# Kernel tuning notes

Hardware: AMD Instinct MI355X
Metric: run time of the kernel (lower is better)

## Reference

```python
import jax, jax.numpy as jnp
import numpy as np


def _compact_positions(mask, K):
    """mask: [B, T] bool. Returns [B, K] with the (ascending) indices t where
    mask[b, t] is True, compacted to the front; remaining slots are -1.
    Stable argsort on ~mask puts True positions first, preserving order.
    """
    order = jnp.argsort(jnp.logical_not(mask), axis=1, stable=True)  # [B, T]
    counts = mask.sum(axis=1, keepdims=True)                          # [B, 1]
    pos = order[:, :K]                                                # [B, K]
    valid = jnp.arange(K)[None, :] < jnp.minimum(counts, K)
    return jnp.where(valid, pos, -1)


def setup_inputs() -> dict:
    key = jax.random.key(0)
    k_r, k_e = jax.random.split(key)
    B, MAX_ROUTING, D = 16, 4096, 512
    routing = jax.random.randint(k_r, (B, MAX_ROUTING), 0, 2, dtype=jnp.int32)
    pos_embed = jax.random.normal(k_e, (MAX_ROUTING, D), dtype=jnp.float32)
    return {"routing": routing, "max_nodes": 1024, "max_edges": 2048,
            "pos_embed": pos_embed}


def reference(routing, max_nodes, max_edges, pos_embed):
    # Compacted logical positions of node tokens (routing==0) and edge tokens
    # (routing==1), replacing the sequential per-batch Python loop.
    node_pos = _compact_positions(routing == 0, max_nodes)  # [B, max_nodes]
    edge_pos = _compact_positions(routing == 1, max_edges)  # [B, max_edges]

    # Each node spans 2 tokens, each edge spans 5 tokens:
    # unsqueeze(-1).repeat(...,k).view == elementwise repeat along axis 1.
    node_tok = jnp.repeat(node_pos, 2, axis=1)  # [B, max_nodes*2]
    edge_tok = jnp.repeat(edge_pos, 5, axis=1)  # [B, max_edges*5]

    node_pe = pos_embed[jnp.maximum(node_tok, 0)]  # [B, max_nodes*2, D]
    edge_pe = pos_embed[jnp.maximum(edge_tok, 0)]  # [B, max_edges*5, D]
    return node_pe, edge_pe
```

## Files before the change

kernel.cpp:

```cpp
#include <hip/hip_runtime.h>

#define NB 16
#define NT 4096
#define ND 512
#define ND4 128
#define MAX_NODES 1024
#define MAX_EDGES 2048
#define NODE_ROWS 2048
#define EDGE_ROWS 10240
#define ROWS_NODE_TOT 32768u
#define ROWS_TOTAL 196608u

typedef __attribute__((ext_vector_type(4))) float f4;

__global__ __launch_bounds__(1024) void compact_kernel(
    const int* __restrict__ routing,
    int* __restrict__ node_pos,
    int* __restrict__ edge_pos)
{
    const int b   = blockIdx.x;
    const int tid = threadIdx.x;
    const int lane = tid & 63;
    const int wv   = tid >> 6;

    const int4 v = reinterpret_cast<const int4*>(routing + b * NT)[tid];
    const int e0 = v.x, e1 = v.y, e2 = v.z, e3 = v.w;

    unsigned inc0 = ((e0 == 0) ? 0x10000u : 0u) | ((e0 == 1) ? 1u : 0u);
    unsigned inc1 = ((e1 == 0) ? 0x10000u : 0u) | ((e1 == 1) ? 1u : 0u);
    unsigned inc2 = ((e2 == 0) ? 0x10000u : 0u) | ((e2 == 1) ? 1u : 0u);
    unsigned inc3 = ((e3 == 0) ? 0x10000u : 0u) | ((e3 == 1) ? 1u : 0u);
    unsigned p0 = inc0;
    unsigned p1 = p0 + inc1;
    unsigned p2 = p1 + inc2;
    unsigned p3 = p2 + inc3;
    const unsigned my_sum = p3;

    unsigned x = my_sum;
    #pragma unroll
    for (int off = 1; off < 64; off <<= 1) {
        unsigned y = __shfl_up(x, off, 64);
        if (lane >= off) x += y;
    }

    __shared__ unsigned wave_sums[16];
    if (lane == 63) wave_sums[wv] = x;

    node_pos[b * MAX_NODES + tid] = -1;
    edge_pos[b * MAX_EDGES + 2 * tid + 0] = -1;
    edge_pos[b * MAX_EDGES + 2 * tid + 1] = -1;
    __syncthreads();

    unsigned offset = 0;
    for (int i = 0; i < wv; ++i) offset += wave_sums[i];

    const unsigned base = offset + x - my_sum;

    const unsigned ex0 = base;
    const unsigned ex1 = base + p0;
    const unsigned ex2 = base + p1;
    const unsigned ex3 = base + p2;

    const int t0 = tid * 4;
    #pragma unroll 4
    for (int i = 0; i < 4; ++i) {
        const int      e  = (i == 0) ? e0 : (i == 1) ? e1 : (i == 2) ? e2 : e3;
        const unsigned ex = (i == 0) ? ex0 : (i == 1) ? ex1 : (i == 2) ? ex2 : ex3;
        if (e == 0) {
            const unsigned rank = ex >> 16;
            if (rank < MAX_NODES) node_pos[b * MAX_NODES + rank] = t0 + i;
        } else if (e == 1) {
            const unsigned rank = ex & 0xFFFFu;
            if (rank < MAX_EDGES) edge_pos[b * MAX_EDGES + rank] = t0 + i;
        }
    }
}

__global__ __launch_bounds__(256) void gather_fused_kernel(
    const float4* __restrict__ pe,
    const int* __restrict__ node_pos,
    const int* __restrict__ edge_pos,
    float4* __restrict__ out)
{
    const unsigned gid = blockIdx.x * 256u + threadIdx.x;
    const unsigned row = gid >> 6;
    const unsigned t   = gid & 63u;

    int tok;
    if (row < ROWS_NODE_TOT) {
        const unsigned b = row >> 11;
        const unsigned j = row & 2047u;
        tok = node_pos[b * MAX_NODES + (j >> 1)];
    } else {
        const unsigned r2 = row - ROWS_NODE_TOT;
        const unsigned b  = r2 / EDGE_ROWS;
        const unsigned j  = r2 - b * EDGE_ROWS;
        tok = edge_pos[b * MAX_EDGES + j / 5u];
    }
    const int src = tok < 0 ? 0 : tok;

    const f4* srcp = (const f4*)(pe + (size_t)src * ND4);
    f4* dstp       = (f4*)(out + (size_t)row * ND4);

    const f4 v0 = srcp[t];
    const f4 v1 = srcp[t + 64];
    __builtin_nontemporal_store(v0, dstp + t);
    __builtin_nontemporal_store(v1, dstp + t + 64);
}

extern "C" void kernel_launch(void* const* d_in, const int* in_sizes, int n_in,
                              void* d_out, int out_size, void* d_ws, size_t ws_size,
                              hipStream_t stream) {
    const int*   routing = (const int*)d_in[0];
    const float* pe      = (const float*)d_in[3];

    int* node_pos = (int*)d_ws;
    int* edge_pos = node_pos + NB * MAX_NODES;

    compact_kernel<<<NB, 1024, 0, stream>>>(routing, node_pos, edge_pos);

    const unsigned total_threads = ROWS_TOTAL * 64u;
    gather_fused_kernel<<<total_threads / 256, 256, 0, stream>>>(
        (const float4*)pe, node_pos, edge_pos, (float4*)d_out);
}
```

Measured before the change: 404.2 us.

## Fuse compaction and gather into one kernel with redundant per-block scan

Merges the compaction kernel and the gather kernel into a single launch. Each of 512 blocks recomputes its batch's prefix-scan compaction into LDS, then gathers its slice of node and edge rows. This removes the second launch, the inter-kernel dependency and the workspace round trip. In exchange, each batch's scan is repeated 32 times, and the grid shrinks to 512 blocks of 1024 threads, which may lower the memory parallelism available for the roughly 400MB write stream.

```diff
diff --git a/kernel.cpp b/kernel.cpp
--- a/kernel.cpp
+++ b/kernel.cpp
@@ -2,26 +2,34 @@
 
 #define NB 16
 #define NT 4096
-#define ND 512
 #define ND4 128
 #define MAX_NODES 1024
 #define MAX_EDGES 2048
 #define NODE_ROWS 2048
 #define EDGE_ROWS 10240
 #define ROWS_NODE_TOT 32768u
-#define ROWS_TOTAL 196608u
+#define SUBS 32
+#define NBLK (NB * SUBS)
+#define NODE_ROWS_PER_BLK 64u
+#define EDGE_ROWS_PER_BLK 320u
 
 typedef __attribute__((ext_vector_type(4))) float f4;
 
-__global__ __launch_bounds__(1024) void compact_kernel(
+__global__ __launch_bounds__(1024) void fused_pe_kernel(
     const int* __restrict__ routing,
-    int* __restrict__ node_pos,
-    int* __restrict__ edge_pos)
+    const f4*  __restrict__ pe,
+    f4*        __restrict__ out)
 {
-    const int b   = blockIdx.x;
-    const int tid = threadIdx.x;
+    const unsigned blk = blockIdx.x;
+    const unsigned b   = blk >> 5;
+    const unsigned sub = blk & 31u;
+    const int tid  = threadIdx.x;
     const int lane = tid & 63;
     const int wv   = tid >> 6;
+
+    __shared__ int      node_lds[MAX_NODES];
+    __shared__ int      edge_lds[MAX_EDGES];
+    __shared__ unsigned wave_sums[16];
 
     const int4 v = reinterpret_cast<const int4*>(routing + b * NT)[tid];
     const int e0 = v.x, e1 = v.y, e2 = v.z, e3 = v.w;
@@ -42,18 +50,15 @@
         unsigned y = __shfl_up(x, off, 64);
         if (lane >= off) x += y;
     }
-
-    __shared__ unsigned wave_sums[16];
     if (lane == 63) wave_sums[wv] = x;
 
-    node_pos[b * MAX_NODES + tid] = -1;
-    edge_pos[b * MAX_EDGES + 2 * tid + 0] = -1;
-    edge_pos[b * MAX_EDGES + 2 * tid + 1] = -1;
+    node_lds[tid]             = -1;
+    edge_lds[2 * tid + 0]     = -1;
+    edge_lds[2 * tid + 1]     = -1;
     __syncthreads();
 
     unsigned offset = 0;
     for (int i = 0; i < wv; ++i) offset += wave_sums[i];
-
     const unsigned base = offset + x - my_sum;
 
     const unsigned ex0 = base;
@@ -68,44 +73,44 @@
         const unsigned ex = (i == 0) ? ex0 : (i == 1) ? ex1 : (i == 2) ? ex2 : ex3;
         if (e == 0) {
             const unsigned rank = ex >> 16;
-            if (rank < MAX_NODES) node_pos[b * MAX_NODES + rank] = t0 + i;
+            if (rank < MAX_NODES) node_lds[rank] = t0 + i;
         } else if (e == 1) {
             const unsigned rank = ex & 0xFFFFu;
-            if (rank < MAX_EDGES) edge_pos[b * MAX_EDGES + rank] = t0 + i;
+            if (rank < MAX_EDGES) edge_lds[rank] = t0 + i;
         }
     }
-}
+    __syncthreads();
 
-__global__ __launch_bounds__(256) void gather_fused_kernel(
-    const float4* __restrict__ pe,
-    const int* __restrict__ node_pos,
-    const int* __restrict__ edge_pos,
-    float4* __restrict__ out)
-{
-    const unsigned gid = blockIdx.x * 256u + threadIdx.x;
-    const unsigned row = gid >> 6;
-    const unsigned t   = gid & 63u;
-
-    int tok;
-    if (row < ROWS_NODE_TOT) {
-        const unsigned b = row >> 11;
-        const unsigned j = row & 2047u;
-        tok = node_pos[b * MAX_NODES + (j >> 1)];
-    } else {
-        const unsigned r2 = row - ROWS_NODE_TOT;
-        const unsigned b  = r2 / EDGE_ROWS;
-        const unsigned j  = r2 - b * EDGE_ROWS;
-        tok = edge_pos[b * MAX_EDGES + j / 5u];
+    {
+        f4* nbase = out + (size_t)b * NODE_ROWS * ND4;
+        #pragma unroll 2
+        for (unsigned r = wv; r < NODE_ROWS_PER_BLK; r += 16) {
+            const unsigned row = sub * NODE_ROWS_PER_BLK + r;
+            const int tok = node_lds[row >> 1];
+            const int src = tok < 0 ? 0 : tok;
+            const f4* s = pe + (size_t)src * ND4;
+            const f4 a0 = s[lane];
+            const f4 a1 = s[lane + 64];
+            f4* d = nbase + (size_t)row * ND4;
+            __builtin_nontemporal_store(a0, d + lane);
+            __builtin_nontemporal_store(a1, d + lane + 64);
+        }
     }
-    const int src = tok < 0 ? 0 : tok;
-
-    const f4* srcp = (const f4*)(pe + (size_t)src * ND4);
-    f4* dstp       = (f4*)(out + (size_t)row * ND4);
-
-    const f4 v0 = srcp[t];
-    const f4 v1 = srcp[t + 64];
-    __builtin_nontemporal_store(v0, dstp + t);
-    __builtin_nontemporal_store(v1, dstp + t + 64);
+    {
+        f4* ebase = out + ((size_t)ROWS_NODE_TOT + (size_t)b * EDGE_ROWS) * ND4;
+        #pragma unroll 4
+        for (unsigned r = wv; r < EDGE_ROWS_PER_BLK; r += 16) {
+            const unsigned row = sub * EDGE_ROWS_PER_BLK + r;
+            const int tok = edge_lds[row / 5u];
+            const int src = tok < 0 ? 0 : tok;
+            const f4* s = pe + (size_t)src * ND4;
+            const f4 a0 = s[lane];
+            const f4 a1 = s[lane + 64];
+            f4* d = ebase + (size_t)row * ND4;
+            __builtin_nontemporal_store(a0, d + lane);
+            __builtin_nontemporal_store(a1, d + lane + 64);
+        }
+    }
 }
 
 extern "C" void kernel_launch(void* const* d_in, const int* in_sizes, int n_in,
@@ -114,12 +119,6 @@
     const int*   routing = (const int*)d_in[0];
     const float* pe      = (const float*)d_in[3];
 
-    int* node_pos = (int*)d_ws;
-    int* edge_pos = node_pos + NB * MAX_NODES;
-
-    compact_kernel<<<NB, 1024, 0, stream>>>(routing, node_pos, edge_pos);
-
-    const unsigned total_threads = ROWS_TOTAL * 64u;
-    gather_fused_kernel<<<total_threads / 256, 256, 0, stream>>>(
-        (const float4*)pe, node_pos, edge_pos, (float4*)d_out);
+    fused_pe_kernel<<<NBLK, 1024, 0, stream>>>(
+        routing, (const f4*)pe, (f4*)d_out);
 }
```

New measurement: 406.8 us. Within noise of the previous version (+0.6%).
